# Kernel optimization log

Measured on AMD Instinct MI355X. Metric: run time of the kernel, lower is better.

Reference implementation:

```python
import jax, jax.numpy as jnp
import numpy as np

C1 = 0.01 ** 2
C2 = 0.03 ** 2
EPS = 1e-8


def _box3(t):
    # 3x3 mean filter, zero padding (SAME), NCHW, 1 channel.
    k = jnp.full((1, 1, 3, 3), 1.0 / 9.0, dtype=t.dtype)
    return jax.lax.conv_general_dilated(
        t, k, window_strides=(1, 1), padding=((1, 1), (1, 1)),
        dimension_numbers=("NCHW", "OIHW", "NCHW"))


def setup_inputs() -> dict:
    key = jax.random.key(0)
    k1, k2 = jax.random.split(key)
    shape = (32, 1, 1024, 1024)
    x = jax.random.uniform(k1, shape, dtype=jnp.float32)
    y = jax.random.uniform(k2, shape, dtype=jnp.float32)
    return {"x": x, "y": y}


def reference(x, y):
    mu_x = _box3(x)
    mu_y = _box3(y)
    sigma_x = _box3(x * x) - mu_x * mu_x
    sigma_y = _box3(y * y) - mu_y * mu_y
    sigma_xy = _box3(x * y) - mu_x * mu_y
    ssim_map = ((2.0 * mu_x * mu_y + C1) * (2.0 * sigma_xy + C2)
                / ((mu_x ** 2 + mu_y ** 2 + C1) * (sigma_x + sigma_y + C2) + EPS))
    return 1.0 - jnp.mean(ssim_map)
```

## Files before the change

### kernel.cpp

```cpp
#include <hip/hip_runtime.h>

#define IMG_H 1024
#define IMG_W 1024
#define RPB   16
#define TPB   256

struct HS { float x[4], y[4], xx[4], yy[4], xy[4]; };

__device__ __forceinline__ void zero_hs(HS& h)
{
#pragma unroll
    for (int j = 0; j < 4; ++j) { h.x[j]=0.f; h.y[j]=0.f; h.xx[j]=0.f; h.yy[j]=0.f; h.xy[j]=0.f; }
}

__device__ __forceinline__ void load_hs(const float* __restrict__ xr,
                                        const float* __restrict__ yr,
                                        int c, HS& h)
{
    float4 xv = *reinterpret_cast<const float4*>(xr + c);
    float4 yv = *reinterpret_cast<const float4*>(yr + c);
    float xs[6], ys[6];
    xs[0] = (c > 0) ? xr[c - 1] : 0.0f;
    ys[0] = (c > 0) ? yr[c - 1] : 0.0f;
    xs[1] = xv.x; xs[2] = xv.y; xs[3] = xv.z; xs[4] = xv.w;
    ys[1] = yv.x; ys[2] = yv.y; ys[3] = yv.z; ys[4] = yv.w;
    xs[5] = (c + 4 < IMG_W) ? xr[c + 4] : 0.0f;
    ys[5] = (c + 4 < IMG_W) ? yr[c + 4] : 0.0f;

    float pxx[6], pyy[6], pxy[6];
#pragma unroll
    for (int k = 0; k < 6; ++k) {
        pxx[k] = xs[k] * xs[k];
        pyy[k] = ys[k] * ys[k];
        pxy[k] = xs[k] * ys[k];
    }
#pragma unroll
    for (int j = 0; j < 4; ++j) {
        h.x[j]  = xs[j]  + xs[j + 1]  + xs[j + 2];
        h.y[j]  = ys[j]  + ys[j + 1]  + ys[j + 2];
        h.xx[j] = pxx[j] + pxx[j + 1] + pxx[j + 2];
        h.yy[j] = pyy[j] + pyy[j + 1] + pyy[j + 2];
        h.xy[j] = pxy[j] + pxy[j + 1] + pxy[j + 2];
    }
}

__device__ __forceinline__ void accum(const HS& A, const HS& B, const HS& C, float& acc)
{
    const float c1s  = 81.0f * 1e-4f;
    const float c2s  = 81.0f * 9e-4f;
    const float epss = 6561.0f * 1e-8f;
#pragma unroll
    for (int j = 0; j < 4; ++j) {
        const float sx  = A.x[j]  + B.x[j]  + C.x[j];
        const float sy  = A.y[j]  + B.y[j]  + C.y[j];
        const float sxx = A.xx[j] + B.xx[j] + C.xx[j];
        const float syy = A.yy[j] + B.yy[j] + C.yy[j];
        const float sxy = A.xy[j] + B.xy[j] + C.xy[j];

        const float t1 = sx * sy;
        const float t2 = fmaf(sx, sx, sy * sy);
        const float s2 = sxx + syy;
        const float An = fmaf(2.0f, t1, c1s);
        const float Bn = fmaf(-2.0f, t1, fmaf(18.0f, sxy, c2s));
        const float Xd = t2 + c1s;
        const float Yd = fmaf(9.0f, s2, c2s - t2);
        const float den = fmaf(Xd, Yd, epss);
        const float num = An * Bn;
        acc = fmaf(num, __builtin_amdgcn_rcpf(den), acc);
    }
}

__global__ __launch_bounds__(TPB)
void ssim_map_sum_kernel(const float* __restrict__ x,
                         const float* __restrict__ y,
                         float* __restrict__ ws_sum)
{
    const int rb = blockIdx.x;
    const int n  = blockIdx.y;
    const int r0 = rb * RPB;
    const int c  = (int)threadIdx.x * 4;

    const float* xi = x + (size_t)n * IMG_H * IMG_W;
    const float* yi = y + (size_t)n * IMG_H * IMG_W;

    HS hA, hB, hC;
    if (r0 > 0) load_hs(xi + (size_t)(r0 - 1) * IMG_W, yi + (size_t)(r0 - 1) * IMG_W, c, hA);
    else        zero_hs(hA);
    load_hs(xi + (size_t)r0 * IMG_W, yi + (size_t)r0 * IMG_W, c, hB);

    float acc = 0.0f;

    for (int i = 0; i < RPB; ++i) {
        const int r = r0 + i;
        if (r + 1 < IMG_H) {
            load_hs(xi + (size_t)(r + 1) * IMG_W, yi + (size_t)(r + 1) * IMG_W, c, hC);
        } else {
            zero_hs(hC);
        }

        accum(hA, hB, hC, acc);

#pragma unroll
        for (int j = 0; j < 4; ++j) {
            hA.x[j]=hB.x[j]; hA.y[j]=hB.y[j]; hA.xx[j]=hB.xx[j]; hA.yy[j]=hB.yy[j]; hA.xy[j]=hB.xy[j];
            hB.x[j]=hC.x[j]; hB.y[j]=hC.y[j]; hB.xx[j]=hC.xx[j]; hB.yy[j]=hC.yy[j]; hB.xy[j]=hC.xy[j];
        }
    }

#pragma unroll
    for (int off = 32; off > 0; off >>= 1)
        acc += __shfl_down(acc, off);

    __shared__ float red[TPB / 64];
    const int lane = (int)threadIdx.x & 63;
    const int wave = (int)threadIdx.x >> 6;
    if (lane == 0) red[wave] = acc;
    __syncthreads();
    if (threadIdx.x == 0) {
        float s = 0.0f;
#pragma unroll
        for (int w = 0; w < TPB / 64; ++w) s += red[w];
        atomicAdd(ws_sum, s);
    }
}

__global__ void ssim_finalize_kernel(const float* __restrict__ ws_sum,
                                     float* __restrict__ out,
                                     float inv_count)
{
    out[0] = 1.0f - ws_sum[0] * inv_count;
}

extern "C" void kernel_launch(void* const* d_in, const int* in_sizes, int n_in,
                              void* d_out, int out_size, void* d_ws, size_t ws_size,
                              hipStream_t stream)
{
    const float* x = (const float*)d_in[0];
    const float* y = (const float*)d_in[1];
    float* out  = (float*)d_out;
    float* wsum = (float*)d_ws;

    const long long total = (long long)in_sizes[0];
    const int N = (int)(total / ((long long)IMG_H * IMG_W));

    hipMemsetAsync(wsum, 0, sizeof(float), stream);

    dim3 grid(IMG_H / RPB, N);
    ssim_map_sum_kernel<<<grid, TPB, 0, stream>>>(x, y, wsum);

    ssim_finalize_kernel<<<1, 1, 0, stream>>>(wsum, out, 1.0f / (float)total);
}
```

Baseline: 297.5 us.

## Unroll row loop with register prefetch, branchless halos, per-block partial sums

Halves rows per block and fully unrolls the eight-row sweep. The next row's float4 loads are issued one step ahead in rotating registers, and edge halos use clamped indices with multiplicative masks instead of branches. The global float atomic is replaced by per-block partial sums that a 256-thread finalize kernel reduces, which also removes the memset. Launch bounds now request 4 blocks per SM, which may limit registers. The smaller row blocks add more vertical halo reloads.

```diff
diff --git a/kernel.cpp b/kernel.cpp
--- a/kernel.cpp
+++ b/kernel.cpp
@@ -2,7 +2,7 @@
 
 #define IMG_H 1024
 #define IMG_W 1024
-#define RPB   16
+#define RPB   8
 #define TPB   256
 
 struct HS { float x[4], y[4], xx[4], yy[4], xy[4]; };
@@ -13,19 +13,11 @@
     for (int j = 0; j < 4; ++j) { h.x[j]=0.f; h.y[j]=0.f; h.xx[j]=0.f; h.yy[j]=0.f; h.xy[j]=0.f; }
 }
 
-__device__ __forceinline__ void load_hs(const float* __restrict__ xr,
-                                        const float* __restrict__ yr,
-                                        int c, HS& h)
-{
-    float4 xv = *reinterpret_cast<const float4*>(xr + c);
-    float4 yv = *reinterpret_cast<const float4*>(yr + c);
-    float xs[6], ys[6];
-    xs[0] = (c > 0) ? xr[c - 1] : 0.0f;
-    ys[0] = (c > 0) ? yr[c - 1] : 0.0f;
-    xs[1] = xv.x; xs[2] = xv.y; xs[3] = xv.z; xs[4] = xv.w;
-    ys[1] = yv.x; ys[2] = yv.y; ys[3] = yv.z; ys[4] = yv.w;
-    xs[5] = (c + 4 < IMG_W) ? xr[c + 4] : 0.0f;
-    ys[5] = (c + 4 < IMG_W) ? yr[c + 4] : 0.0f;
+__device__ __forceinline__ void hsum6(float xl, float4 xv, float xr6,
+                                      float yl, float4 yv, float yr6, HS& h)
+{
+    float xs[6] = { xl, xv.x, xv.y, xv.z, xv.w, xr6 };
+    float ys[6] = { yl, yv.x, yv.y, yv.z, yv.w, yr6 };
 
     float pxx[6], pyy[6], pxy[6];
 #pragma unroll
@@ -70,41 +62,90 @@
     }
 }
 
-__global__ __launch_bounds__(TPB)
+__global__ __launch_bounds__(TPB, 4)
 void ssim_map_sum_kernel(const float* __restrict__ x,
                          const float* __restrict__ y,
-                         float* __restrict__ ws_sum)
+                         float* __restrict__ part)
 {
     const int rb = blockIdx.x;
     const int n  = blockIdx.y;
     const int r0 = rb * RPB;
     const int c  = (int)threadIdx.x * 4;
 
+    const int   cl = (c > 0) ? c - 1 : 0;
+    const int   cr = (c + 4 < IMG_W) ? c + 4 : IMG_W - 1;
+    const float lm = (c > 0) ? 1.0f : 0.0f;
+    const float rm = (c + 4 < IMG_W) ? 1.0f : 0.0f;
+
     const float* xi = x + (size_t)n * IMG_H * IMG_W;
     const float* yi = y + (size_t)n * IMG_H * IMG_W;
 
     HS hA, hB, hC;
-    if (r0 > 0) load_hs(xi + (size_t)(r0 - 1) * IMG_W, yi + (size_t)(r0 - 1) * IMG_W, c, hA);
-    else        zero_hs(hA);
-    load_hs(xi + (size_t)r0 * IMG_W, yi + (size_t)r0 * IMG_W, c, hB);
+
+    if (r0 > 0) {
+        const float* xr = xi + (size_t)(r0 - 1) * IMG_W;
+        const float* yr = yi + (size_t)(r0 - 1) * IMG_W;
+        hsum6(xr[cl] * lm, *reinterpret_cast<const float4*>(xr + c), xr[cr] * rm,
+              yr[cl] * lm, *reinterpret_cast<const float4*>(yr + c), yr[cr] * rm, hA);
+    } else {
+        zero_hs(hA);
+    }
+    {
+        const float* xr = xi + (size_t)r0 * IMG_W;
+        const float* yr = yi + (size_t)r0 * IMG_W;
+        hsum6(xr[cl] * lm, *reinterpret_cast<const float4*>(xr + c), xr[cr] * rm,
+              yr[cl] * lm, *reinterpret_cast<const float4*>(yr + c), yr[cr] * rm, hB);
+    }
+
+    float4 pxa = *reinterpret_cast<const float4*>(xi + (size_t)(r0 + 1) * IMG_W + c);
+    float4 pya = *reinterpret_cast<const float4*>(yi + (size_t)(r0 + 1) * IMG_W + c);
+    float4 pxb, pyb;
 
     float acc = 0.0f;
 
-    for (int i = 0; i < RPB; ++i) {
-        const int r = r0 + i;
-        if (r + 1 < IMG_H) {
-            load_hs(xi + (size_t)(r + 1) * IMG_W, yi + (size_t)(r + 1) * IMG_W, c, hC);
-        } else {
-            zero_hs(hC);
-        }
-
+#define STEP_MAIN(k, PXI, PYI, PXO, PYO, P, Q, R)                                  \
+    {                                                                              \
+        const float* xw = xi + (size_t)(r0 + (k) + 2) * IMG_W;                     \
+        const float* yw = yi + (size_t)(r0 + (k) + 2) * IMG_W;                     \
+        PXO = *reinterpret_cast<const float4*>(xw + c);                            \
+        PYO = *reinterpret_cast<const float4*>(yw + c);                            \
+        const float* xu = xi + (size_t)(r0 + (k) + 1) * IMG_W;                     \
+        const float* yu = yi + (size_t)(r0 + (k) + 1) * IMG_W;                     \
+        hsum6(xu[cl] * lm, PXI, xu[cr] * rm, yu[cl] * lm, PYI, yu[cr] * rm, R);    \
+        accum(P, Q, R, acc);                                                       \
+    }
+
+    STEP_MAIN(0, pxa, pya, pxb, pyb, hA, hB, hC)
+    STEP_MAIN(1, pxb, pyb, pxa, pya, hB, hC, hA)
+    STEP_MAIN(2, pxa, pya, pxb, pyb, hC, hA, hB)
+    STEP_MAIN(3, pxb, pyb, pxa, pya, hA, hB, hC)
+    STEP_MAIN(4, pxa, pya, pxb, pyb, hB, hC, hA)
+    STEP_MAIN(5, pxb, pyb, pxa, pya, hC, hA, hB)
+#undef STEP_MAIN
+
+    {
+        const int rr = (r0 + 8 < IMG_H) ? r0 + 8 : IMG_H - 1;
+        const float* xw = xi + (size_t)rr * IMG_W;
+        const float* yw = yi + (size_t)rr * IMG_W;
+        pxb = *reinterpret_cast<const float4*>(xw + c);
+        pyb = *reinterpret_cast<const float4*>(yw + c);
+        const float* xu = xi + (size_t)(r0 + 7) * IMG_W;
+        const float* yu = yi + (size_t)(r0 + 7) * IMG_W;
+        hsum6(xu[cl] * lm, pxa, xu[cr] * rm, yu[cl] * lm, pya, yu[cr] * rm, hC);
         accum(hA, hB, hC, acc);
-
-#pragma unroll
-        for (int j = 0; j < 4; ++j) {
-            hA.x[j]=hB.x[j]; hA.y[j]=hB.y[j]; hA.xx[j]=hB.xx[j]; hA.yy[j]=hB.yy[j]; hA.xy[j]=hB.xy[j];
-            hB.x[j]=hC.x[j]; hB.y[j]=hC.y[j]; hB.xx[j]=hC.xx[j]; hB.yy[j]=hC.yy[j]; hB.xy[j]=hC.xy[j];
-        }
+    }
+
+    {
+        const float rwm = (r0 + 8 < IMG_H) ? 1.0f : 0.0f;
+        const int rr = (r0 + 8 < IMG_H) ? r0 + 8 : IMG_H - 1;
+        const float* xu = xi + (size_t)rr * IMG_W;
+        const float* yu = yi + (size_t)rr * IMG_W;
+        float4 xv = pxb, yv = pyb;
+        xv.x *= rwm; xv.y *= rwm; xv.z *= rwm; xv.w *= rwm;
+        yv.x *= rwm; yv.y *= rwm; yv.z *= rwm; yv.w *= rwm;
+        hsum6(xu[cl] * (lm * rwm), xv, xu[cr] * (rm * rwm),
+              yu[cl] * (lm * rwm), yv, yu[cr] * (rm * rwm), hA);
+        accum(hB, hC, hA, acc);
     }
 
 #pragma unroll
@@ -120,15 +161,30 @@
         float s = 0.0f;
 #pragma unroll
         for (int w = 0; w < TPB / 64; ++w) s += red[w];
-        atomicAdd(ws_sum, s);
-    }
-}
-
-__global__ void ssim_finalize_kernel(const float* __restrict__ ws_sum,
-                                     float* __restrict__ out,
-                                     float inv_count)
-{
-    out[0] = 1.0f - ws_sum[0] * inv_count;
+        part[blockIdx.y * gridDim.x + blockIdx.x] = s;
+    }
+}
+
+__global__ __launch_bounds__(256)
+void ssim_finalize_kernel(const float* __restrict__ part, int nparts,
+                          float* __restrict__ out, float inv_count)
+{
+    float s = 0.0f;
+    for (int i = (int)threadIdx.x; i < nparts; i += 256)
+        s += part[i];
+#pragma unroll
+    for (int off = 32; off > 0; off >>= 1)
+        s += __shfl_down(s, off);
+
+    __shared__ float red[4];
+    const int lane = (int)threadIdx.x & 63;
+    const int wave = (int)threadIdx.x >> 6;
+    if (lane == 0) red[wave] = s;
+    __syncthreads();
+    if (threadIdx.x == 0) {
+        float t = red[0] + red[1] + red[2] + red[3];
+        out[0] = 1.0f - t * inv_count;
+    }
 }
 
 extern "C" void kernel_launch(void* const* d_in, const int* in_sizes, int n_in,
@@ -138,15 +194,14 @@
     const float* x = (const float*)d_in[0];
     const float* y = (const float*)d_in[1];
     float* out  = (float*)d_out;
-    float* wsum = (float*)d_ws;
+    float* part = (float*)d_ws;
 
     const long long total = (long long)in_sizes[0];
     const int N = (int)(total / ((long long)IMG_H * IMG_W));
-
-    hipMemsetAsync(wsum, 0, sizeof(float), stream);
+    const int nparts = (IMG_H / RPB) * N;
 
     dim3 grid(IMG_H / RPB, N);
-    ssim_map_sum_kernel<<<grid, TPB, 0, stream>>>(x, y, wsum);
-
-    ssim_finalize_kernel<<<1, 1, 0, stream>>>(wsum, out, 1.0f / (float)total);
-}
+    ssim_map_sum_kernel<<<grid, TPB, 0, stream>>>(x, y, part);
+
+    ssim_finalize_kernel<<<1, 256, 0, stream>>>(part, nparts, out, 1.0f / (float)total);
+}
```

Measured after the change: 277.0 us. 1.07x faster.
